# Optimization experiments

Hardware: AMD Instinct MI355X
Metric: run time of the kernel (lower is better)

The kernel has to match this reference:

```python
import jax, jax.numpy as jnp
import numpy as np

N_NODES = 50000


def _glorot(key, fan_in, fan_out):
    lim = jnp.sqrt(6.0 / (fan_in + fan_out)).astype(jnp.float32)
    return jax.random.uniform(key, (fan_in, fan_out), jnp.float32, -lim, lim)


def gcn_layer(x, W, b, src, dst, deg_inv_sqrt):
    # PyG GCNConv: x' = D^{-1/2} (A + I) D^{-1/2} (x W) + b
    h = x @ W  # [N, F_out]
    norm = deg_inv_sqrt[src] * deg_inv_sqrt[dst]  # [E+N]
    msg = norm[:, None] * h[src]                  # gather + scale
    out = jax.ops.segment_sum(msg, dst, num_segments=x.shape[0])
    return out + b


def setup_inputs() -> dict:
    key = jax.random.key(0)
    ks = jax.random.split(key, 8)
    in_c, out_c = 128, 64
    hid = 2 * out_c
    x = jax.random.normal(ks[0], (N_NODES, in_c), jnp.float32)
    edge_index = jax.random.randint(ks[1], (2, 800000), 0, N_NODES, jnp.int64)
    return {
        "x": x,
        "edge_index": edge_index,
        "W1": _glorot(ks[2], in_c, hid), "b1": jnp.zeros((hid,), jnp.float32),
        "W2": _glorot(ks[3], hid, hid),  "b2": jnp.zeros((hid,), jnp.float32),
        "W3": _glorot(ks[4], hid, out_c), "b3": jnp.zeros((out_c,), jnp.float32),
    }


def reference(x, edge_index, W1, b1, W2, b2, W3, b3):
    n = x.shape[0]
    loops = jnp.arange(n, dtype=edge_index.dtype)
    src = jnp.concatenate([edge_index[0], loops])  # [E+N]
    dst = jnp.concatenate([edge_index[1], loops])
    deg = jax.ops.segment_sum(jnp.ones_like(dst, dtype=x.dtype), dst, num_segments=n)
    deg_inv_sqrt = jnp.where(deg > 0, jax.lax.rsqrt(deg), 0.0)

    h = jax.nn.relu(gcn_layer(x, W1, b1, src, dst, deg_inv_sqrt))
    h = jax.nn.relu(gcn_layer(h, W2, b2, src, dst, deg_inv_sqrt))
    return gcn_layer(h, W3, b3, src, dst, deg_inv_sqrt)
```

## Files before the change

### kernel.cpp

```cpp
#include <hip/hip_runtime.h>
#include <hip/hip_bf16.h>
#include <hip/hip_fp16.h>
#include <cstdint>
#include <cstddef>

typedef _Float16 half8_t __attribute__((ext_vector_type(8)));
typedef float f32x4 __attribute__((ext_vector_type(4)));


__global__ __launch_bounds__(256) void prep_kernel(int* __restrict__ cnt, int N4,
                                                   const float* __restrict__ W1, _Float16* __restrict__ wt1,
                                                   const float* __restrict__ W2, _Float16* __restrict__ wt2,
                                                   const float* __restrict__ W3, _Float16* __restrict__ wt3) {
  int i = blockIdx.x * 256 + threadIdx.x;
  if (i < N4) {
    *(int4*)&cnt[i * 4] = make_int4(0, 0, 0, 0);
    return;
  }
  int j = i - N4;
  if (j < 16384) {
    int k = j >> 7, c = j & 127;
    wt1[c * 128 + k] = (_Float16)W1[j];
    return;
  }
  j -= 16384;
  if (j < 16384) {
    int k = j >> 7, c = j & 127;
    wt2[c * 128 + k] = (_Float16)W2[j];
    return;
  }
  j -= 16384;
  if (j < 8192) {
    int k = j >> 6, c = j & 63;
    wt3[c * 128 + k] = (_Float16)W3[j];
  }
}


__global__ __launch_bounds__(256) void countpos_kernel(const int* __restrict__ dst,
                                                       int* __restrict__ cnt,
                                                       ushort* __restrict__ pos, int E) {
  int e = (blockIdx.x * blockDim.x + threadIdx.x) * 4;
  if (e + 4 <= E) {
    int4 d = *(const int4*)&dst[e];
    int p0 = atomicAdd(&cnt[d.x], 1);
    int p1 = atomicAdd(&cnt[d.y], 1);
    int p2 = atomicAdd(&cnt[d.z], 1);
    int p3 = atomicAdd(&cnt[d.w], 1);
    ushort4 pk;
    pk.x = (ushort)p0; pk.y = (ushort)p1; pk.z = (ushort)p2; pk.w = (ushort)p3;
    *(ushort4*)&pos[e] = pk;
  } else {
    for (; e < E; ++e) pos[e] = (ushort)atomicAdd(&cnt[dst[e]], 1);
  }
}

__global__ __launch_bounds__(256) void block_sum_kernel(const int* __restrict__ cnt,
                                                        int* __restrict__ bsum, int N) {
  const int tid = threadIdx.x, lane = tid & 63, wid = tid >> 6;
  __shared__ int wt[4];
  int base = blockIdx.x * 2048 + tid * 8;
  int s = 0;
#pragma unroll
  for (int q = 0; q < 8; ++q) { int i = base + q; if (i < N) s += cnt[i]; }
#pragma unroll
  for (int off = 32; off; off >>= 1) s += __shfl_down(s, off);
  if (lane == 0) wt[wid] = s;
  __syncthreads();
  if (tid == 0) bsum[blockIdx.x] = wt[0] + wt[1] + wt[2] + wt[3];
}

__global__ __launch_bounds__(256) void scan_bsum_kernel(const int* __restrict__ bsum,
                                                        int* __restrict__ boff,
                                                        int NB, int E, int* __restrict__ rpN) {
  __shared__ int sh[256];
  const int tid = threadIdx.x;
  int v = (tid < NB) ? bsum[tid] : 0;
  sh[tid] = v;
  __syncthreads();
  for (int off = 1; off < 256; off <<= 1) {
    int t = (tid >= off) ? sh[tid - off] : 0;
    __syncthreads();
    sh[tid] += t;
    __syncthreads();
  }
  if (tid < NB) boff[tid] = sh[tid] - v;
  if (tid == 0) rpN[0] = E;
}

__global__ __launch_bounds__(256) void scan_apply_kernel(const int* __restrict__ cnt,
                                                         const int* __restrict__ boff,
                                                         int* __restrict__ rp,
                                                         float* __restrict__ dis, int N) {
  const int tid = threadIdx.x, lane = tid & 63, wid = tid >> 6;
  __shared__ int wtot[4], wexc[4];
  int base = blockIdx.x * 2048 + tid * 8;
  int v[8]; int s = 0;
#pragma unroll
  for (int q = 0; q < 8; ++q) { int i = base + q; int x = (i < N) ? cnt[i] : 0; v[q] = x; s += x; }
  int sc = s;
#pragma unroll
  for (int off = 1; off < 64; off <<= 1) { int t = __shfl_up(sc, off); if (lane >= off) sc += t; }
  if (lane == 63) wtot[wid] = sc;
  __syncthreads();
  if (tid == 0) { int r = 0; for (int wq = 0; wq < 4; ++wq) { wexc[wq] = r; r += wtot[wq]; } }
  __syncthreads();
  int thr = boff[blockIdx.x] + wexc[wid] + (sc - s);
#pragma unroll
  for (int q = 0; q < 8; ++q) {
    int i = base + q;
    if (i < N) { rp[i] = thr; dis[i] = rsqrtf((float)(v[q] + 1)); }
    thr += v[q];
  }
}


__global__ __launch_bounds__(256) void place_gemm1_kernel(const int* __restrict__ src,
                                                          const int* __restrict__ dst,
                                                          const ushort* __restrict__ pos,
                                                          const int* __restrict__ rp,
                                                          ushort* __restrict__ ss, int E,
                                                          const float* __restrict__ X,
                                                          const half8_t* __restrict__ Wt,
                                                          const float* __restrict__ dis,
                                                          _Float16* __restrict__ G, int N,
                                                          int gemmBlocks) {
  if (blockIdx.x >= gemmBlocks) {
    int e = ((blockIdx.x - gemmBlocks) * blockDim.x + threadIdx.x) * 4;
    if (e + 4 <= E) {
      int4 d = *(const int4*)&dst[e];
      ushort4 p = *(const ushort4*)&pos[e];
      int4 s = *(const int4*)&src[e];
      int r0 = rp[d.x], r1 = rp[d.y], r2 = rp[d.z], r3 = rp[d.w];
      ss[r0 + p.x] = (ushort)s.x;
      ss[r1 + p.y] = (ushort)s.y;
      ss[r2 + p.z] = (ushort)s.z;
      ss[r3 + p.w] = (ushort)s.w;
    } else {
      for (; e < E; ++e) ss[rp[dst[e]] + pos[e]] = (ushort)src[e];
    }
    return;
  }
  const int wave = threadIdx.x >> 6;
  const int lane = threadIdx.x & 63;
  const int wm = wave >> 1, wn = wave & 1;
  const int row0 = blockIdx.x * 128 + wm * 64;
  const int col0 = wn * 64;
  const int lr = lane & 15;
  const int lk = lane >> 4;
  f32x4 acc[4][4];
#pragma unroll
  for (int r = 0; r < 4; ++r)
#pragma unroll
    for (int c = 0; c < 4; ++c) acc[r][c] = (f32x4){0.f, 0.f, 0.f, 0.f};

#pragma unroll
  for (int ks = 0; ks < 4; ++ks) {
    half8_t a[4], b[4];
#pragma unroll
    for (int r = 0; r < 4; ++r) {
      int row = row0 + r * 16 + lr;
      half8_t av = {};
      if (row < N) {
        const float* xp = &X[(size_t)row * 128 + ks * 32 + lk * 8];
        float4 xa = *(const float4*)xp;
        float4 xb = *(const float4*)(xp + 4);
        av[0] = (_Float16)xa.x; av[1] = (_Float16)xa.y; av[2] = (_Float16)xa.z; av[3] = (_Float16)xa.w;
        av[4] = (_Float16)xb.x; av[5] = (_Float16)xb.y; av[6] = (_Float16)xb.z; av[7] = (_Float16)xb.w;
      }
      a[r] = av;
    }
#pragma unroll
    for (int c = 0; c < 4; ++c) {
      int col = col0 + c * 16 + lr;
      b[c] = Wt[(size_t)col * 16 + ks * 4 + lk];
    }
#pragma unroll
    for (int r = 0; r < 4; ++r)
#pragma unroll
      for (int c = 0; c < 4; ++c)
        acc[r][c] = __builtin_amdgcn_mfma_f32_16x16x32_f16(a[r], b[c], acc[r][c], 0, 0, 0);
  }

#pragma unroll
  for (int r = 0; r < 4; ++r) {
#pragma unroll
    for (int q = 0; q < 4; ++q) {
      int row = row0 + r * 16 + lk * 4 + q;
      if (row < N) {
        float dv = dis[row];
#pragma unroll
        for (int c = 0; c < 4; ++c)
          G[(size_t)row * 128 + col0 + c * 16 + lr] = (_Float16)(acc[r][c][q] * dv);
      }
    }
  }
}


template <int COUT>
__global__ __launch_bounds__(256) void fused_agg_gemm_kernel(const _Float16* __restrict__ G,
                                                             const int* __restrict__ rp,
                                                             const ushort* __restrict__ ss,
                                                             const float* __restrict__ dis,
                                                             const float* __restrict__ bias,
                                                             const half8_t* __restrict__ Wt,
                                                             _Float16* __restrict__ G2, int N) {
  __shared__ _Float16 sh[32][136];
  const int wave = threadIdx.x >> 6;
  const int lane = threadIdx.x & 63;
  const int grp = lane >> 4;
  const int sub = lane & 15;
  const int nb0 = blockIdx.x * 32;

#pragma unroll
  for (int it = 0; it < 2; ++it) {
    const int wl = it * 16 + wave * 4 + grp;
    const int w = nb0 + wl;
    if (w < N) {
      const int e0 = rp[w], e1 = rp[w + 1];
      float acc[8];
      half8_t sv = *(const half8_t*)&G[(size_t)w * 128 + sub * 8];
#pragma unroll
      for (int j = 0; j < 8; ++j) acc[j] = (float)sv[j];
      int e = e0;
      for (; e + 8 <= e1; e += 8) {
        int jj[8];
#pragma unroll
        for (int q = 0; q < 8; ++q) jj[q] = ss[e + q];
        half8_t v[8];
#pragma unroll
        for (int q = 0; q < 8; ++q) v[q] = *(const half8_t*)&G[(size_t)jj[q] * 128 + sub * 8];
#pragma unroll
        for (int j = 0; j < 8; ++j)
          acc[j] += (((float)v[0][j] + (float)v[1][j]) + ((float)v[2][j] + (float)v[3][j])) +
                    (((float)v[4][j] + (float)v[5][j]) + ((float)v[6][j] + (float)v[7][j]));
      }
      for (; e + 2 <= e1; e += 2) {
        int i0 = ss[e], i1 = ss[e + 1];
        half8_t v0 = *(const half8_t*)&G[(size_t)i0 * 128 + sub * 8];
        half8_t v1 = *(const half8_t*)&G[(size_t)i1 * 128 + sub * 8];
#pragma unroll
        for (int j = 0; j < 8; ++j) acc[j] += (float)v0[j] + (float)v1[j];
      }
      for (; e < e1; ++e) {
        half8_t v0 = *(const half8_t*)&G[(size_t)ss[e] * 128 + sub * 8];
#pragma unroll
        for (int j = 0; j < 8; ++j) acc[j] += (float)v0[j];
      }
      float d = dis[w];
      float4 b0 = *(const float4*)&bias[sub * 8];
      float4 b1 = *(const float4*)&bias[sub * 8 + 4];
      float bb[8] = {b0.x, b0.y, b0.z, b0.w, b1.x, b1.y, b1.z, b1.w};
      half8_t o;
#pragma unroll
      for (int j = 0; j < 8; ++j) {
        float v = fmaxf(d * acc[j] + bb[j], 0.f);
        o[j] = (_Float16)v;
      }
      *(half8_t*)&sh[wl][sub * 8] = o;
    }
  }
  __syncthreads();

  const int lr = lane & 15;
  const int lk = lane >> 4;
  constexpr int NC = COUT / 64;
  const int col0 = wave * (COUT / 4);
  f32x4 acc2[2][NC];
#pragma unroll
  for (int r = 0; r < 2; ++r)
#pragma unroll
    for (int c = 0; c < NC; ++c) acc2[r][c] = (f32x4){0.f, 0.f, 0.f, 0.f};

#pragma unroll
  for (int ks = 0; ks < 4; ++ks) {
    half8_t a[2], b[NC];
#pragma unroll
    for (int r = 0; r < 2; ++r)
      a[r] = *(const half8_t*)&sh[r * 16 + lr][ks * 32 + lk * 8];
#pragma unroll
    for (int c = 0; c < NC; ++c) {
      int col = col0 + c * 16 + lr;
      b[c] = Wt[(size_t)col * 16 + ks * 4 + lk];
    }
#pragma unroll
    for (int r = 0; r < 2; ++r)
#pragma unroll
      for (int c = 0; c < NC; ++c)
        acc2[r][c] = __builtin_amdgcn_mfma_f32_16x16x32_f16(a[r], b[c], acc2[r][c], 0, 0, 0);
  }

#pragma unroll
  for (int r = 0; r < 2; ++r) {
#pragma unroll
    for (int q = 0; q < 4; ++q) {
      int row = nb0 + r * 16 + lk * 4 + q;
      if (row < N) {
        float dv = dis[row];
#pragma unroll
        for (int c = 0; c < NC; ++c)
          G2[(size_t)row * COUT + col0 + c * 16 + lr] = (_Float16)(acc2[r][c][q] * dv);
      }
    }
  }
}


__global__ __launch_bounds__(256) void agg64_kernel(const _Float16* __restrict__ G,
                                                    const int* __restrict__ rp,
                                                    const ushort* __restrict__ ss,
                                                    const float* __restrict__ dis,
                                                    const float* __restrict__ bias,
                                                    float* __restrict__ OUT, int N) {
  const int wave = threadIdx.x >> 6;
  const int lane = threadIdx.x & 63;
  const int grp = lane >> 3;
  const int sub = lane & 7;
  const int w = blockIdx.x * 32 + wave * 8 + grp;
  if (w >= N) return;
  const int e0 = rp[w], e1 = rp[w + 1];
  float acc[8];
  half8_t sv = *(const half8_t*)&G[(size_t)w * 64 + sub * 8];
#pragma unroll
  for (int j = 0; j < 8; ++j) acc[j] = (float)sv[j];
  int e = e0;
  for (; e + 8 <= e1; e += 8) {
    int jj[8];
#pragma unroll
    for (int q = 0; q < 8; ++q) jj[q] = ss[e + q];
    half8_t v[8];
#pragma unroll
    for (int q = 0; q < 8; ++q) v[q] = *(const half8_t*)&G[(size_t)jj[q] * 64 + sub * 8];
#pragma unroll
    for (int j = 0; j < 8; ++j)
      acc[j] += (((float)v[0][j] + (float)v[1][j]) + ((float)v[2][j] + (float)v[3][j])) +
                (((float)v[4][j] + (float)v[5][j]) + ((float)v[6][j] + (float)v[7][j]));
  }
  for (; e + 2 <= e1; e += 2) {
    int i0 = ss[e], i1 = ss[e + 1];
    half8_t v0 = *(const half8_t*)&G[(size_t)i0 * 64 + sub * 8];
    half8_t v1 = *(const half8_t*)&G[(size_t)i1 * 64 + sub * 8];
#pragma unroll
    for (int j = 0; j < 8; ++j) acc[j] += (float)v0[j] + (float)v1[j];
  }
  for (; e < e1; ++e) {
    half8_t v0 = *(const half8_t*)&G[(size_t)ss[e] * 64 + sub * 8];
#pragma unroll
    for (int j = 0; j < 8; ++j) acc[j] += (float)v0[j];
  }
  float d = dis[w];
  float4 b0 = *(const float4*)&bias[sub * 8];
  float4 b1 = *(const float4*)&bias[sub * 8 + 4];
  float4 o0, o1;
  o0.x = d * acc[0] + b0.x; o0.y = d * acc[1] + b0.y;
  o0.z = d * acc[2] + b0.z; o0.w = d * acc[3] + b0.w;
  o1.x = d * acc[4] + b1.x; o1.y = d * acc[5] + b1.y;
  o1.z = d * acc[6] + b1.z; o1.w = d * acc[7] + b1.w;
  *(float4*)&OUT[(size_t)w * 64 + sub * 8] = o0;
  *(float4*)&OUT[(size_t)w * 64 + sub * 8 + 4] = o1;
}


extern "C" void kernel_launch(void* const* d_in, const int* in_sizes, int n_in,
                              void* d_out, int out_size, void* d_ws, size_t ws_size,
                              hipStream_t stream) {
  const float* x  = (const float*)d_in[0];
  const int*   ei = (const int*)d_in[1];
  const float* W1 = (const float*)d_in[2];
  const float* b1 = (const float*)d_in[3];
  const float* W2 = (const float*)d_in[4];
  const float* b2 = (const float*)d_in[5];
  const float* W3 = (const float*)d_in[6];
  const float* b3 = (const float*)d_in[7];

  const int inC = in_sizes[2] / in_sizes[3];
  const int N = in_sizes[0] / inC;
  const int E = in_sizes[1] / 2;

  auto align256 = [](size_t v) { return (v + 255) & ~(size_t)255; };
  char* p = (char*)d_ws;
  int* cnt = (int*)p;   p += align256((size_t)N * 4);
  int* rp  = (int*)p;   p += align256((size_t)(N + 1) * 4);
  ushort* ss = (ushort*)p;  p += align256((size_t)E * 2);
  ushort* pos = (ushort*)p; p += align256((size_t)E * 2);
  float* dis = (float*)p; p += align256((size_t)N * 4);
  _Float16* gA = (_Float16*)p; p += align256((size_t)N * 128 * 2);
  _Float16* gB = (_Float16*)p; p += align256((size_t)N * 128 * 2);
  _Float16* wt1 = (_Float16*)p; p += align256((size_t)128 * 128 * 2);
  _Float16* wt2 = (_Float16*)p; p += align256((size_t)128 * 128 * 2);
  _Float16* wt3 = (_Float16*)p; p += align256((size_t)64 * 128 * 2);
  int* bsum = (int*)p;  p += align256(1024 * 4);
  int* boff = (int*)p;  p += align256(1024 * 4);

  const int* srcv = ei;
  const int* dstv = ei + E;

  const int NB = (N + 2047) / 2048;
  const int eB4 = (E / 4 + 255) / 256;
  const int N4 = (N + 3) / 4;
  const int prepTot = N4 + 16384 + 16384 + 8192;

  prep_kernel<<<(prepTot + 255) / 256, 256, 0, stream>>>(cnt, N4, W1, wt1, W2, wt2, W3, wt3);
  countpos_kernel<<<eB4, 256, 0, stream>>>(dstv, cnt, pos, E);
  block_sum_kernel<<<NB, 256, 0, stream>>>(cnt, bsum, N);
  scan_bsum_kernel<<<1, 256, 0, stream>>>(bsum, boff, NB, E, rp + N);
  scan_apply_kernel<<<NB, 256, 0, stream>>>(cnt, boff, rp, dis, N);

  const int g1B = (N + 127) / 128;
  const int fB  = (N + 31) / 32;
  const int a64B = (N + 31) / 32;

  place_gemm1_kernel<<<g1B + eB4, 256, 0, stream>>>(srcv, dstv, pos, rp, ss, E,
                                                    x, (const half8_t*)wt1, dis, gA, N, g1B);
  fused_agg_gemm_kernel<128><<<fB, 256, 0, stream>>>(gA, rp, ss, dis, b1, (const half8_t*)wt2, gB, N);
  fused_agg_gemm_kernel<64><<<fB, 256, 0, stream>>>(gB, rp, ss, dis, b2, (const half8_t*)wt3, gA, N);
  agg64_kernel<<<a64B, 256, 0, stream>>>(gA, rp, ss, dis, b3, (float*)d_out, N);
}
```

Baseline: 177.8 us.

## Pad CSR rows to multiples of eight with zero-row sentinel for vector index loads

Each destination's neighbor list is padded up to a multiple of 8 entries. The padding is filled with a sentinel index N that points to an extra zero row appended to each feature buffer. The aggregation loops then read indices as one 16-byte vector and drop their 2-wide and scalar remainder loops, which removes divergent tails. In exchange they gather extra zero rows (about 3.5 extra per node on average), fill the index array up front, and need a separate gC buffer because gA has no spare zero row layout for 64-wide data.

Result: faster. 169.3 us (-4.8%).

```diff
diff --git a/kernel.cpp b/kernel.cpp
--- a/kernel.cpp
+++ b/kernel.cpp
@@ -6,12 +6,15 @@
 
 typedef _Float16 half8_t __attribute__((ext_vector_type(8)));
 typedef float f32x4 __attribute__((ext_vector_type(4)));
+typedef unsigned short ushort8_v __attribute__((ext_vector_type(8)));
 
 
 __global__ __launch_bounds__(256) void prep_kernel(int* __restrict__ cnt, int N4,
                                                    const float* __restrict__ W1, _Float16* __restrict__ wt1,
                                                    const float* __restrict__ W2, _Float16* __restrict__ wt2,
-                                                   const float* __restrict__ W3, _Float16* __restrict__ wt3) {
+                                                   const float* __restrict__ W3, _Float16* __restrict__ wt3,
+                                                   _Float16* __restrict__ gA, _Float16* __restrict__ gB,
+                                                   _Float16* __restrict__ gC, int N) {
   int i = blockIdx.x * 256 + threadIdx.x;
   if (i < N4) {
     *(int4*)&cnt[i * 4] = make_int4(0, 0, 0, 0);
@@ -33,13 +36,29 @@
   if (j < 8192) {
     int k = j >> 6, c = j & 63;
     wt3[c * 128 + k] = (_Float16)W3[j];
-  }
-}
-
-
-__global__ __launch_bounds__(256) void countpos_kernel(const int* __restrict__ dst,
-                                                       int* __restrict__ cnt,
-                                                       ushort* __restrict__ pos, int E) {
+    return;
+  }
+  j -= 8192;
+  if (j < 40) {
+    half8_t z = {};
+    if (j < 16)       *(half8_t*)&gA[(size_t)N * 128 + j * 8] = z;
+    else if (j < 32)  *(half8_t*)&gB[(size_t)N * 128 + (j - 16) * 8] = z;
+    else              *(half8_t*)&gC[(size_t)N * 64 + (j - 32) * 8] = z;
+  }
+}
+
+
+__global__ __launch_bounds__(256) void countpos_fill_kernel(const int* __restrict__ dst,
+                                                            int* __restrict__ cnt,
+                                                            ushort* __restrict__ pos, int E,
+                                                            int* __restrict__ ssInt, int ssInts,
+                                                            int countBlocks, int fillPat) {
+  if (blockIdx.x >= countBlocks) {
+    int f = ((blockIdx.x - countBlocks) * 256 + threadIdx.x) * 4;
+    if (f + 4 <= ssInts) *(int4*)&ssInt[f] = make_int4(fillPat, fillPat, fillPat, fillPat);
+    else for (; f < ssInts; ++f) ssInt[f] = fillPat;
+    return;
+  }
   int e = (blockIdx.x * blockDim.x + threadIdx.x) * 4;
   if (e + 4 <= E) {
     int4 d = *(const int4*)&dst[e];
@@ -62,7 +81,7 @@
   int base = blockIdx.x * 2048 + tid * 8;
   int s = 0;
 #pragma unroll
-  for (int q = 0; q < 8; ++q) { int i = base + q; if (i < N) s += cnt[i]; }
+  for (int q = 0; q < 8; ++q) { int i = base + q; if (i < N) s += (cnt[i] + 7) & ~7; }
 #pragma unroll
   for (int off = 32; off; off >>= 1) s += __shfl_down(s, off);
   if (lane == 0) wt[wid] = s;
@@ -72,7 +91,7 @@
 
 __global__ __launch_bounds__(256) void scan_bsum_kernel(const int* __restrict__ bsum,
                                                         int* __restrict__ boff,
-                                                        int NB, int E, int* __restrict__ rpN) {
+                                                        int NB, int* __restrict__ rpN) {
   __shared__ int sh[256];
   const int tid = threadIdx.x;
   int v = (tid < NB) ? bsum[tid] : 0;
@@ -85,7 +104,7 @@
     __syncthreads();
   }
   if (tid < NB) boff[tid] = sh[tid] - v;
-  if (tid == 0) rpN[0] = E;
+  if (tid == 255) rpN[0] = sh[255];
 }
 
 __global__ __launch_bounds__(256) void scan_apply_kernel(const int* __restrict__ cnt,
@@ -97,7 +116,10 @@
   int base = blockIdx.x * 2048 + tid * 8;
   int v[8]; int s = 0;
 #pragma unroll
-  for (int q = 0; q < 8; ++q) { int i = base + q; int x = (i < N) ? cnt[i] : 0; v[q] = x; s += x; }
+  for (int q = 0; q < 8; ++q) {
+    int i = base + q; int x = (i < N) ? cnt[i] : 0;
+    v[q] = x; s += (x + 7) & ~7;
+  }
   int sc = s;
 #pragma unroll
   for (int off = 1; off < 64; off <<= 1) { int t = __shfl_up(sc, off); if (lane >= off) sc += t; }
@@ -110,7 +132,7 @@
   for (int q = 0; q < 8; ++q) {
     int i = base + q;
     if (i < N) { rp[i] = thr; dis[i] = rsqrtf((float)(v[q] + 1)); }
-    thr += v[q];
+    thr += (v[q] + 7) & ~7;
   }
 }
 
@@ -223,30 +245,15 @@
       half8_t sv = *(const half8_t*)&G[(size_t)w * 128 + sub * 8];
 #pragma unroll
       for (int j = 0; j < 8; ++j) acc[j] = (float)sv[j];
-      int e = e0;
-      for (; e + 8 <= e1; e += 8) {
-        int jj[8];
-#pragma unroll
-        for (int q = 0; q < 8; ++q) jj[q] = ss[e + q];
+      for (int e = e0; e < e1; e += 8) {
+        ushort8_v iv = *(const ushort8_v*)&ss[e];
         half8_t v[8];
 #pragma unroll
-        for (int q = 0; q < 8; ++q) v[q] = *(const half8_t*)&G[(size_t)jj[q] * 128 + sub * 8];
+        for (int q = 0; q < 8; ++q) v[q] = *(const half8_t*)&G[(size_t)iv[q] * 128 + sub * 8];
 #pragma unroll
         for (int j = 0; j < 8; ++j)
           acc[j] += (((float)v[0][j] + (float)v[1][j]) + ((float)v[2][j] + (float)v[3][j])) +
                     (((float)v[4][j] + (float)v[5][j]) + ((float)v[6][j] + (float)v[7][j]));
-      }
-      for (; e + 2 <= e1; e += 2) {
-        int i0 = ss[e], i1 = ss[e + 1];
-        half8_t v0 = *(const half8_t*)&G[(size_t)i0 * 128 + sub * 8];
-        half8_t v1 = *(const half8_t*)&G[(size_t)i1 * 128 + sub * 8];
-#pragma unroll
-        for (int j = 0; j < 8; ++j) acc[j] += (float)v0[j] + (float)v1[j];
-      }
-      for (; e < e1; ++e) {
-        half8_t v0 = *(const half8_t*)&G[(size_t)ss[e] * 128 + sub * 8];
-#pragma unroll
-        for (int j = 0; j < 8; ++j) acc[j] += (float)v0[j];
       }
       float d = dis[w];
       float4 b0 = *(const float4*)&bias[sub * 8];
@@ -324,30 +331,15 @@
   half8_t sv = *(const half8_t*)&G[(size_t)w * 64 + sub * 8];
 #pragma unroll
   for (int j = 0; j < 8; ++j) acc[j] = (float)sv[j];
-  int e = e0;
-  for (; e + 8 <= e1; e += 8) {
-    int jj[8];
-#pragma unroll
-    for (int q = 0; q < 8; ++q) jj[q] = ss[e + q];
+  for (int e = e0; e < e1; e += 8) {
+    ushort8_v iv = *(const ushort8_v*)&ss[e];
     half8_t v[8];
 #pragma unroll
-    for (int q = 0; q < 8; ++q) v[q] = *(const half8_t*)&G[(size_t)jj[q] * 64 + sub * 8];
+    for (int q = 0; q < 8; ++q) v[q] = *(const half8_t*)&G[(size_t)iv[q] * 64 + sub * 8];
 #pragma unroll
     for (int j = 0; j < 8; ++j)
       acc[j] += (((float)v[0][j] + (float)v[1][j]) + ((float)v[2][j] + (float)v[3][j])) +
                 (((float)v[4][j] + (float)v[5][j]) + ((float)v[6][j] + (float)v[7][j]));
-  }
-  for (; e + 2 <= e1; e += 2) {
-    int i0 = ss[e], i1 = ss[e + 1];
-    half8_t v0 = *(const half8_t*)&G[(size_t)i0 * 64 + sub * 8];
-    half8_t v1 = *(const half8_t*)&G[(size_t)i1 * 64 + sub * 8];
-#pragma unroll
-    for (int j = 0; j < 8; ++j) acc[j] += (float)v0[j] + (float)v1[j];
-  }
-  for (; e < e1; ++e) {
-    half8_t v0 = *(const half8_t*)&G[(size_t)ss[e] * 64 + sub * 8];
-#pragma unroll
-    for (int j = 0; j < 8; ++j) acc[j] += (float)v0[j];
   }
   float d = dis[w];
   float4 b0 = *(const float4*)&bias[sub * 8];
@@ -378,15 +370,18 @@
   const int N = in_sizes[0] / inC;
   const int E = in_sizes[1] / 2;
 
+  const int SSPAD = ((E + 7 * N + 8) + 7) & ~7;
+
   auto align256 = [](size_t v) { return (v + 255) & ~(size_t)255; };
   char* p = (char*)d_ws;
   int* cnt = (int*)p;   p += align256((size_t)N * 4);
   int* rp  = (int*)p;   p += align256((size_t)(N + 1) * 4);
-  ushort* ss = (ushort*)p;  p += align256((size_t)E * 2);
+  ushort* ss = (ushort*)p;  p += align256((size_t)SSPAD * 2);
   ushort* pos = (ushort*)p; p += align256((size_t)E * 2);
   float* dis = (float*)p; p += align256((size_t)N * 4);
-  _Float16* gA = (_Float16*)p; p += align256((size_t)N * 128 * 2);
-  _Float16* gB = (_Float16*)p; p += align256((size_t)N * 128 * 2);
+  _Float16* gA = (_Float16*)p; p += align256((size_t)(N + 1) * 128 * 2);
+  _Float16* gB = (_Float16*)p; p += align256((size_t)(N + 1) * 128 * 2);
+  _Float16* gC = (_Float16*)p; p += align256((size_t)(N + 1) * 64 * 2);
   _Float16* wt1 = (_Float16*)p; p += align256((size_t)128 * 128 * 2);
   _Float16* wt2 = (_Float16*)p; p += align256((size_t)128 * 128 * 2);
   _Float16* wt3 = (_Float16*)p; p += align256((size_t)64 * 128 * 2);
@@ -399,12 +394,17 @@
   const int NB = (N + 2047) / 2048;
   const int eB4 = (E / 4 + 255) / 256;
   const int N4 = (N + 3) / 4;
-  const int prepTot = N4 + 16384 + 16384 + 8192;
-
-  prep_kernel<<<(prepTot + 255) / 256, 256, 0, stream>>>(cnt, N4, W1, wt1, W2, wt2, W3, wt3);
-  countpos_kernel<<<eB4, 256, 0, stream>>>(dstv, cnt, pos, E);
+  const int prepTot = N4 + 16384 + 16384 + 8192 + 40;
+  const int ssInts = SSPAD / 2;
+  const int fillB = (ssInts / 4 + 255) / 256;
+  const int fillPat = (int)(((unsigned)N) | (((unsigned)N) << 16));
+
+  prep_kernel<<<(prepTot + 255) / 256, 256, 0, stream>>>(cnt, N4, W1, wt1, W2, wt2, W3, wt3,
+                                                         gA, gB, gC, N);
+  countpos_fill_kernel<<<eB4 + fillB, 256, 0, stream>>>(dstv, cnt, pos, E,
+                                                        (int*)ss, ssInts, eB4, fillPat);
   block_sum_kernel<<<NB, 256, 0, stream>>>(cnt, bsum, N);
-  scan_bsum_kernel<<<1, 256, 0, stream>>>(bsum, boff, NB, E, rp + N);
+  scan_bsum_kernel<<<1, 256, 0, stream>>>(bsum, boff, NB, rp + N);
   scan_apply_kernel<<<NB, 256, 0, stream>>>(cnt, boff, rp, dis, N);
 
   const int g1B = (N + 127) / 128;
@@ -414,6 +414,6 @@
   place_gemm1_kernel<<<g1B + eB4, 256, 0, stream>>>(srcv, dstv, pos, rp, ss, E,
                                                     x, (const half8_t*)wt1, dis, gA, N, g1B);
   fused_agg_gemm_kernel<128><<<fB, 256, 0, stream>>>(gA, rp, ss, dis, b1, (const half8_t*)wt2, gB, N);
-  fused_agg_gemm_kernel<64><<<fB, 256, 0, stream>>>(gB, rp, ss, dis, b2, (const half8_t*)wt3, gA, N);
-  agg64_kernel<<<a64B, 256, 0, stream>>>(gA, rp, ss, dis, b3, (float*)d_out, N);
-}
+  fused_agg_gemm_kernel<64><<<fB, 256, 0, stream>>>(gB, rp, ss, dis, b2, (const half8_t*)wt3, gC, N);
+  agg64_kernel<<<a64B, 256, 0, stream>>>(gC, rp, ss, dis, b3, (float*)d_out, N);
+}
```
